# Performance work log

Measured on AMD Instinct MI355X. Metric: run time of the kernel, lower is better.

The kernel has to match this reference:

```python
import jax, jax.numpy as jnp
import numpy as np

B, N, S = 8, 4096, 1024
D1, D2 = 128, 256
IN_C = D1 + D2
MLP = [256, 256]
BN_EPS = 1e-5


def setup_inputs() -> dict:
    key = jax.random.key(0)
    ks = jax.random.split(key, 32)
    inp = {
        'xyz1': jax.random.uniform(ks[0], (B, 3, N), dtype=jnp.float32),
        'xyz2': jax.random.uniform(ks[1], (B, 3, S), dtype=jnp.float32),
        'points1': jax.random.normal(ks[2], (B, D1, N), dtype=jnp.float32),
        'points2': jax.random.normal(ks[3], (B, D2, S), dtype=jnp.float32),
        'colors1': jax.random.normal(ks[4], (B, D1, N), dtype=jnp.float32),
        'colors2': jax.random.normal(ks[5], (B, D2, S), dtype=jnp.float32),
    }
    # conv1x1 + BN params for the two MLP stacks (points / colors)
    k = 6
    last = IN_C
    for li, out_c in enumerate(MLP, start=1):
        for tag in ('p', 'c'):
            scale = 1.0 / np.sqrt(last)
            inp[f'W{tag}{li}'] = jax.random.uniform(ks[k], (out_c, last), jnp.float32, -scale, scale); k += 1
            inp[f'b{tag}{li}'] = jax.random.uniform(ks[k], (out_c,), jnp.float32, -scale, scale); k += 1
            inp[f'g{tag}{li}'] = jnp.ones((out_c,), jnp.float32)
            inp[f'be{tag}{li}'] = jnp.zeros((out_c,), jnp.float32)
        last = out_c
    return inp


def _square_distance(src, dst):
    # src [B,N,3], dst [B,S,3] -> [B,N,S]
    d = -2.0 * jnp.einsum('bnc,bsc->bns', src, dst)
    d = d + jnp.sum(src * src, -1)[:, :, None]
    d = d + jnp.sum(dst * dst, -1)[:, None, :]
    return d


def _three_interp(xyz1, xyz2, feat2):
    # xyz1 [B,N,3], xyz2 [B,S,3], feat2 [B,S,D] -> [B,N,D]
    dists = _square_distance(xyz1, xyz2)              # [B,N,S]
    neg_d3, idx = jax.lax.top_k(-dists, 3)            # smallest 3 distances
    d3 = -neg_d3                                      # [B,N,3] ascending
    recip = 1.0 / (d3 + 1e-8)
    weight = recip / jnp.sum(recip, axis=2, keepdims=True)
    gathered = jax.vmap(lambda f, i: f[i])(feat2, idx)  # [B,N,3,D]
    return jnp.sum(gathered * weight[..., None], axis=2)


def _conv_bn_relu(x, W, b, g, be):
    # x [B,N,Cin]; conv1x1 == per-point linear; BN in training mode (batch stats)
    y = jnp.einsum('bnc,oc->bno', x, W) + b
    m = jnp.mean(y, axis=(0, 1))
    v = jnp.var(y, axis=(0, 1))
    yn = (y - m) * jax.lax.rsqrt(v + BN_EPS)
    return jax.nn.relu(yn * g + be)


def reference(xyz1, xyz2, points1, points2, colors1, colors2,
              Wp1, bp1, gp1, bep1, Wc1, bc1, gc1, bec1,
              Wp2, bp2, gp2, bep2, Wc2, bc2, gc2, bec2):
    x1 = jnp.transpose(xyz1, (0, 2, 1))   # [B,N,3]
    x2 = jnp.transpose(xyz2, (0, 2, 1))   # [B,S,3]
    p2 = jnp.transpose(points2, (0, 2, 1))  # [B,S,D2]
    c2 = jnp.transpose(colors2, (0, 2, 1))

    interp_p = _three_interp(x1, x2, p2)  # [B,N,D2]
    interp_c = _three_interp(x1, x2, c2)

    p1 = jnp.transpose(points1, (0, 2, 1))  # [B,N,D1]
    c1 = jnp.transpose(colors1, (0, 2, 1))
    new_p = jnp.concatenate([p1, interp_p], axis=-1)  # [B,N,IN_C]
    new_c = jnp.concatenate([c1, interp_c], axis=-1)

    new_p = _conv_bn_relu(new_p, Wp1, bp1, gp1, bep1)
    new_p = _conv_bn_relu(new_p, Wp2, bp2, gp2, bep2)
    new_c = _conv_bn_relu(new_c, Wc1, bc1, gc1, bec1)
    new_c = _conv_bn_relu(new_c, Wc2, bc2, gc2, bec2)

    return (jnp.transpose(new_p, (0, 2, 1)), jnp.transpose(new_c, (0, 2, 1)))
```

## Files before the change

kernel.cpp:

```cpp
#include <hip/hip_runtime.h>
#include <cstdint>
#include <cstddef>


#define B_   8
#define N_   4096
#define S_   1024
#define D1_  128
#define D2_  256
#define INC_ 384
#define OC_  256
#define M_   (B_ * N_)

typedef __attribute__((ext_vector_type(8))) short sh8;
typedef __attribute__((ext_vector_type(4))) float f32x4;
typedef __attribute__((ext_vector_type(4))) unsigned short ush4;
typedef __attribute__((ext_vector_type(8))) unsigned short ush8;

__device__ __forceinline__ unsigned short bf16rne(float f) {
    union { float f; unsigned u; } v; v.f = f;
    return (unsigned short)((v.u + 0x7FFFu + ((v.u >> 16) & 1u)) >> 16);
}
__device__ __forceinline__ float bf2f(unsigned short h) {
    union { unsigned u; float f; } v; v.u = ((unsigned)h) << 16;
    return v.f;
}
__device__ __forceinline__ void gload16(const void* gsrc, void* lds) {
    __builtin_amdgcn_global_load_lds(
        (const __attribute__((address_space(1))) void*)gsrc,
        (__attribute__((address_space(3))) void*)lds, 16, 0, 0);
}

#define INS(pd, pi) { \
    bool l0 = (pd < d0) || (pd == d0 && pi < i0); \
    bool l1 = (pd < d1) || (pd == d1 && pi < i1); \
    bool l2 = (pd < d2) || (pd == d2 && pi < i2); \
    d2 = l1 ? d1 : (l2 ? pd : d2);  i2 = l1 ? i1 : (l2 ? pi : i2); \
    d1 = l0 ? d0 : (l1 ? pd : d1);  i1 = l0 ? i0 : (l1 ? pi : i1); \
    d0 = l0 ? pd : d0;              i0 = l0 ? pi : i0; \
}

__global__ __launch_bounds__(256) void front_kernel(
    const float* __restrict__ xyz1, const float* __restrict__ xyz2,
    const float* __restrict__ points1, const float* __restrict__ colors1,
    const float* __restrict__ points2, const float* __restrict__ colors2,
    const float* __restrict__ Wp1, const float* __restrict__ Wc1,
    const float* __restrict__ Wp2, const float* __restrict__ Wc2,
    int* __restrict__ idxo, float* __restrict__ wo,
    unsigned short* __restrict__ p2b, unsigned short* __restrict__ c2b,
    unsigned short* __restrict__ Wb1, unsigned short* __restrict__ Wb2,
    unsigned short* __restrict__ Xp)
{
    __shared__ __align__(16) char fsm[17664];
    const int bid = blockIdx.x;
    const int tid = threadIdx.x;

    if (bid < 1024) {
        float4* sc = (float4*)fsm;
        const int b = bid >> 7, qb = bid & 127;
        const float* x2 = xyz2 + (size_t)b * 3 * S_;
        for (int s = tid; s < S_; s += 256) {
            float xs = x2[s], ys = x2[S_ + s], zs = x2[2 * S_ + s];
            sc[s] = make_float4(xs, ys, zs, xs * xs + ys * ys + zs * zs);
        }
        __syncthreads();
        const int q = qb * 32 + (tid >> 3);
        const int sub = tid & 7;
        const float* x1 = xyz1 + (size_t)b * 3 * N_;
        const float xq = x1[q], yq = x1[N_ + q], zq = x1[2 * N_ + q];
        const float n1 = xq * xq + yq * yq + zq * zq;
        float d0 = 3.4e38f, d1 = 3.4e38f, d2 = 3.4e38f;
        int i0 = 0, i1 = 0, i2 = 0;
#pragma unroll 4
        for (int j = 0; j < 128; ++j) {
            int s = j * 8 + sub;
            float4 v = sc[s];
            float dot = xq * v.x + yq * v.y + zq * v.z;
            float d = (n1 - 2.0f * dot) + v.w;
            bool c0 = d < d0, c1 = d < d1, c2 = d < d2;
            d2 = c1 ? d1 : (c2 ? d : d2); i2 = c1 ? i1 : (c2 ? s : i2);
            d1 = c0 ? d0 : (c1 ? d : d1); i1 = c0 ? i0 : (c1 ? s : i1);
            d0 = c0 ? d : d0;             i0 = c0 ? s : i0;
        }
#pragma unroll
        for (int off = 1; off < 8; off <<= 1) {
            float pd0 = __shfl_xor(d0, off), pd1 = __shfl_xor(d1, off), pd2 = __shfl_xor(d2, off);
            int   pi0 = __shfl_xor(i0, off), pi1 = __shfl_xor(i1, off), pi2 = __shfl_xor(i2, off);
            INS(pd0, pi0) INS(pd1, pi1) INS(pd2, pi2)
        }
        if (sub == 0) {
            float r0 = 1.f / (d0 + 1e-8f);
            float r1 = 1.f / (d1 + 1e-8f);
            float r2 = 1.f / (d2 + 1e-8f);
            float rs = r0 + r1 + r2;
            int base = (b * N_ + q) * 3;
            idxo[base] = i0; idxo[base + 1] = i1; idxo[base + 2] = i2;
            wo[base] = r0 / rs; wo[base + 1] = r1 / rs; wo[base + 2] = r2 / rs;
        }
    } else if (bid < 1536) {
        float (*tile)[33] = (float(*)[33])fsm;
        const int u = bid - 1024;
        const int which = u >> 8;
        const int v = u & 255;
        const int z = v >> 5, cx = v & 31;
        const int tx = tid & 31, ty = tid >> 5;
        const float* s = (which ? colors2 : points2) + (size_t)z * D2_ * S_;
        unsigned short* d = (which ? c2b : p2b) + (size_t)z * S_ * D2_;
        for (int ry = 0; ry < 8; ++ry) {
            if (ry) __syncthreads();
#pragma unroll
            for (int i = 0; i < 4; ++i)
                tile[ty + i * 8][tx] = s[(size_t)(ry * 32 + ty + i * 8) * S_ + cx * 32 + tx];
            __syncthreads();
#pragma unroll
            for (int i = 0; i < 4; ++i)
                d[(size_t)(cx * 32 + ty + i * 8) * D2_ + ry * 32 + tx] =
                    bf16rne(tile[tx][ty + i * 8]);
        }
    } else if (bid < 1856) {
        int e = ((bid - 1536) * 256 + tid) * 4;
        const float* src; unsigned short* dst; int off;
        if (e < 98304)       { src = Wp1; dst = Wb1;          off = e; }
        else if (e < 196608) { src = Wc1; dst = Wb1 + 98304;  off = e - 98304; }
        else if (e < 262144) { src = Wp2; dst = Wb2;          off = e - 196608; }
        else                 { src = Wc2; dst = Wb2 + 65536;  off = e - 262144; }
        float4 v = *(const float4*)(src + off);
        ush4 o; o[0] = bf16rne(v.x); o[1] = bf16rne(v.y); o[2] = bf16rne(v.z); o[3] = bf16rne(v.w);
        *(ush4*)(dst + off) = o;
    } else {
        float (*tileA)[69] = (float(*)[69])fsm;
        const int u = bid - 1856;
        const int t = u >> 9, rem = u & 511;
        const int b = rem >> 6, n0 = (rem & 63) * 64;
        const float* x1 = t ? colors1 : points1;
        size_t mbase = (size_t)t * M_ + (size_t)b * N_ + n0;
#pragma unroll
        for (int ph = 0; ph < 2; ++ph) {
            if (ph) __syncthreads();
#pragma unroll
            for (int it = 0; it < 4; ++it) {
                int fl4 = it * 256 + tid;
                int dl = fl4 >> 4, nl = (fl4 & 15) * 4;
                float4 v = *(const float4*)(x1 + ((size_t)b * D1_ + ph * 64 + dl) * N_ + n0 + nl);
                tileA[nl][dl] = v.x; tileA[nl + 1][dl] = v.y;
                tileA[nl + 2][dl] = v.z; tileA[nl + 3][dl] = v.w;
            }
            __syncthreads();
#pragma unroll
            for (int it = 0; it < 2; ++it) {
                int e8 = it * 256 + tid;
                int r = e8 >> 3, dc = (e8 & 7) * 8;
                ush8 o;
#pragma unroll
                for (int j = 0; j < 8; ++j) o[j] = bf16rne(tileA[r][dc + j]);
                *(ush8*)(Xp + (mbase + r) * D1_ + ph * 64 + dc) = o;
            }
        }
    }
}

__global__ __launch_bounds__(512, 1) void gemm1f_kernel(
    const unsigned short* __restrict__ Xp,
    const unsigned short* __restrict__ p2b,
    const unsigned short* __restrict__ c2b,
    const int* __restrict__ idxw, const float* __restrict__ wgtw,
    const unsigned short* __restrict__ Wb1,
    unsigned short* __restrict__ Y1,
    float* __restrict__ psum, float* __restrict__ psq)
{
    const int wg  = blockIdx.x;
    const int xcd = wg & 7;
    const int t   = xcd & 1;
    const int mt  = (xcd >> 1) * 32 + (wg >> 3);
    const int m0  = mt * 256;
    const int bb  = m0 >> 12;
    const unsigned short* Aw  = Wb1 + (size_t)t * (OC_ * INC_);
    const unsigned short* Xb  = Xp + (size_t)t * M_ * D1_;
    const unsigned short* f2b = t ? c2b : p2b;

    __shared__ __align__(16) char smem[131072];

    const int tid  = threadIdx.x;
    const int lane = tid & 63;
    const int wid  = tid >> 6;
    const int wc   = wid & 3;
    const int wm   = wid >> 2;
    const int srow = tid >> 3;
    const int k8   = (tid & 7) * 8;
    const int sk   = ((tid & 7) ^ (srow & 7)) * 8;
    const int kgrp = (lane >> 4) * 16;

    int gi[4][3]; float gw[4][3];
#pragma unroll
    for (int p = 0; p < 4; ++p) {
        int base = (m0 + p * 64 + srow) * 3;
#pragma unroll
        for (int j = 0; j < 3; ++j) { gi[p][j] = idxw[base + j]; gw[p][j] = wgtw[base + j]; }
    }

    f32x4 acc[4][8];
#pragma unroll
    for (int i = 0; i < 4; ++i)
#pragma unroll
        for (int j = 0; j < 8; ++j) acc[i][j] = f32x4{0.f, 0.f, 0.f, 0.f};

    auto stageA = [&](int buf, int kc) {
#pragma unroll
        for (int p = 0; p < 4; ++p)
            gload16(Aw + (size_t)(p * 64 + srow) * INC_ + kc + sk,
                    smem + buf * 32768 + p * 8192 + wid * 1024);
    };
    auto stageBX = [&](int buf, int kc) {
#pragma unroll
        for (int p = 0; p < 4; ++p)
            gload16(Xb + (size_t)(m0 + p * 64 + srow) * D1_ + kc + sk,
                    smem + 65536 + buf * 32768 + p * 8192 + wid * 1024);
    };
    auto stageBG = [&](int buf, int kc) {
        const int d0k = kc - D1_ + k8;
#pragma unroll
        for (int p = 0; p < 4; ++p) {
            int row = p * 64 + srow;
            ush8 a0 = *(const ush8*)(f2b + ((size_t)bb * S_ + gi[p][0]) * D2_ + d0k);
            ush8 a1 = *(const ush8*)(f2b + ((size_t)bb * S_ + gi[p][1]) * D2_ + d0k);
            ush8 a2 = *(const ush8*)(f2b + ((size_t)bb * S_ + gi[p][2]) * D2_ + d0k);
            ush8 ov;
#pragma unroll
            for (int j = 0; j < 8; ++j)
                ov[j] = bf16rne(gw[p][0] * bf2f(a0[j]) + gw[p][1] * bf2f(a1[j])
                              + gw[p][2] * bf2f(a2[j]));
            *(ush8*)(smem + 65536 + buf * 32768 + row * 128
                     + ((k8 * 2) ^ ((row & 7) << 4))) = ov;
        }
    };
    auto compute = [&](int buf) {
#pragma unroll
        for (int kk = 0; kk < 2; ++kk) {
            sh8 a[4], b[8];
#pragma unroll
            for (int f = 0; f < 4; ++f) {
                int ra = wc * 64 + (lane & 15) + f * 16;
                a[f] = *(const sh8*)(smem + buf * 32768 + ra * 128
                        + ((kk * 64 + kgrp) ^ ((ra & 7) << 4)));
            }
#pragma unroll
            for (int f = 0; f < 8; ++f) {
                int rb = wm * 128 + (lane & 15) + f * 16;
                b[f] = *(const sh8*)(smem + 65536 + buf * 32768 + rb * 128
                        + ((kk * 64 + kgrp) ^ ((rb & 7) << 4)));
            }
#pragma unroll
            for (int fc = 0; fc < 4; ++fc)
#pragma unroll
                for (int fm = 0; fm < 8; ++fm)
                    acc[fc][fm] = __builtin_amdgcn_mfma_f32_16x16x32_bf16(
                        a[fc], b[fm], acc[fc][fm], 0, 0, 0);
        }
    };

    stageA(0, 0); stageBX(0, 0);
    __syncthreads();
    int cur = 0;
    for (int step = 0; step < 6; ++step) {
        int kcn = (step + 1) * 64;
        if (step < 5) {
            stageA(cur ^ 1, kcn);
            if (kcn < D1_) stageBX(cur ^ 1, kcn);
            else           stageBG(cur ^ 1, kcn);
        }
        compute(cur);
        __syncthreads();
        cur ^= 1;
    }

    const int mrow = m0 + wm * 128 + (lane & 15);
    const int chq  = (lane >> 4) * 4;
#pragma unroll
    for (int fm = 0; fm < 8; ++fm)
#pragma unroll
        for (int fc = 0; fc < 4; ++fc) {
            ush4 v;
#pragma unroll
            for (int r = 0; r < 4; ++r) v[r] = bf16rne(acc[fc][fm][r]);
            *(ush4*)(Y1 + ((size_t)t * M_ + mrow + fm * 16) * OC_
                      + wc * 64 + fc * 16 + chq) = v;
        }

    float* sArr = (float*)smem;
    const int contrib = wm * 16 + (lane & 15);
#pragma unroll
    for (int ph = 0; ph < 2; ++ph) {
#pragma unroll
        for (int fc = 0; fc < 4; ++fc) {
            f32x4 s4;
#pragma unroll
            for (int r = 0; r < 4; ++r) {
                float s = 0.f;
#pragma unroll
                for (int fm = 0; fm < 8; ++fm) { float v = acc[fc][fm][r]; s += ph ? v * v : v; }
                s4[r] = s;
            }
            *(f32x4*)&sArr[contrib * 264 + wc * 64 + fc * 16 + chq] = s4;
        }
        __syncthreads();
        if (tid < 256) {
            float s = 0.f;
#pragma unroll
            for (int k = 0; k < 32; ++k) s += sArr[((k + tid) & 31) * 264 + tid];
            (ph ? psq : psum)[((size_t)t * 128 + mt) * 256 + tid] = s;
        }
        __syncthreads();
    }
}

__global__ __launch_bounds__(256) void reduce_kernel(
    const float* __restrict__ psum, const float* __restrict__ psq,
    const float* __restrict__ gp, const float* __restrict__ bep,
    const float* __restrict__ gc, const float* __restrict__ bec,
    float* __restrict__ ss, int layerOff)
{
    const int t = blockIdx.x, cs = blockIdx.y;
    const int tid = threadIdx.x;
    const int cl = tid & 63, grp = tid >> 6;
    const int c = cs * 64 + cl;
    float s = 0.f, q = 0.f;
    for (int k = grp; k < 128; k += 4) {
        s += psum[((size_t)t * 128 + k) * 256 + c];
        q += psq [((size_t)t * 128 + k) * 256 + c];
    }
    __shared__ float ls[4][64], lq[4][64];
    ls[grp][cl] = s; lq[grp][cl] = q;
    __syncthreads();
    if (tid < 64) {
        s = ls[0][cl] + ls[1][cl] + ls[2][cl] + ls[3][cl];
        q = lq[0][cl] + lq[1][cl] + lq[2][cl] + lq[3][cl];
        float mean = s * (1.f / (float)M_);
        float var  = q * (1.f / (float)M_) - mean * mean;
        float inv  = rsqrtf(var + 1e-5f);
        float g = (t ? gc : gp)[c], be = (t ? bec : bep)[c];
        float sc = g * inv;
        ss[layerOff + t * 256 + c]       = sc;
        ss[layerOff + 512 + t * 256 + c] = be - mean * sc;
    }
}

__global__ __launch_bounds__(512, 1) void gemm2f_kernel(
    const unsigned short* __restrict__ Y1,
    const unsigned short* __restrict__ Wb2,
    const float* __restrict__ ss,
    unsigned short* __restrict__ y2b,
    float* __restrict__ psum, float* __restrict__ psq)
{
    const int wg  = blockIdx.x;
    const int xcd = wg & 7;
    const int t   = xcd & 1;
    const int mt  = (xcd >> 1) * 32 + (wg >> 3);
    const int m0  = mt * 256;
    const unsigned short* Aw = Wb2 + (size_t)t * (OC_ * OC_);
    const unsigned short* By = Y1 + (size_t)t * M_ * OC_;

    __shared__ __align__(16) char smem[131072];
    __shared__ float Slds[256], Hlds[256];

    const int tid  = threadIdx.x;
    const int lane = tid & 63;
    const int wid  = tid >> 6;
    const int wc   = wid & 3;
    const int wm   = wid >> 2;
    const int srow = tid >> 3;
    const int k8   = (tid & 7) * 8;
    const int sk   = ((tid & 7) ^ (srow & 7)) * 8;
    const int kgrp = (lane >> 4) * 16;

    if (tid < 256) { Slds[tid] = ss[t * 256 + tid]; Hlds[tid] = ss[512 + t * 256 + tid]; }
    __syncthreads();

    f32x4 acc[4][8];
#pragma unroll
    for (int i = 0; i < 4; ++i)
#pragma unroll
        for (int j = 0; j < 8; ++j) acc[i][j] = f32x4{0.f, 0.f, 0.f, 0.f};

    auto stageA = [&](int buf, int kc) {
#pragma unroll
        for (int p = 0; p < 4; ++p)
            gload16(Aw + (size_t)(p * 64 + srow) * OC_ + kc + sk,
                    smem + buf * 32768 + p * 8192 + wid * 1024);
    };
    auto stageBY = [&](int buf, int kc) {
#pragma unroll
        for (int p = 0; p < 4; ++p) {
            int row = p * 64 + srow;
            ush8 yv = *(const ush8*)(By + (size_t)(m0 + row) * OC_ + kc + k8);
            ush8 ov;
#pragma unroll
            for (int j = 0; j < 8; ++j) {
                float y = bf2f(yv[j]);
                ov[j] = bf16rne(fmaxf(0.f, fmaf(y, Slds[kc + k8 + j], Hlds[kc + k8 + j])));
            }
            *(ush8*)(smem + 65536 + buf * 32768 + row * 128
                     + ((k8 * 2) ^ ((row & 7) << 4))) = ov;
        }
    };
    auto compute = [&](int buf) {
#pragma unroll
        for (int kk = 0; kk < 2; ++kk) {
            sh8 a[4], b[8];
#pragma unroll
            for (int f = 0; f < 4; ++f) {
                int ra = wc * 64 + (lane & 15) + f * 16;
                a[f] = *(const sh8*)(smem + buf * 32768 + ra * 128
                        + ((kk * 64 + kgrp) ^ ((ra & 7) << 4)));
            }
#pragma unroll
            for (int f = 0; f < 8; ++f) {
                int rb = wm * 128 + (lane & 15) + f * 16;
                b[f] = *(const sh8*)(smem + 65536 + buf * 32768 + rb * 128
                        + ((kk * 64 + kgrp) ^ ((rb & 7) << 4)));
            }
#pragma unroll
            for (int fc = 0; fc < 4; ++fc)
#pragma unroll
                for (int fm = 0; fm < 8; ++fm)
                    acc[fc][fm] = __builtin_amdgcn_mfma_f32_16x16x32_bf16(
                        a[fc], b[fm], acc[fc][fm], 0, 0, 0);
        }
    };

    stageA(0, 0); stageBY(0, 0);
    __syncthreads();
    int cur = 0;
    for (int step = 0; step < 4; ++step) {
        int kcn = (step + 1) * 64;
        if (step < 3) { stageA(cur ^ 1, kcn); stageBY(cur ^ 1, kcn); }
        compute(cur);
        __syncthreads();
        cur ^= 1;
    }

    const int mrow = m0 + wm * 128 + (lane & 15);
    const int chq  = (lane >> 4) * 4;
#pragma unroll
    for (int fm = 0; fm < 8; ++fm)
#pragma unroll
        for (int fc = 0; fc < 4; ++fc) {
            ush4 v;
#pragma unroll
            for (int r = 0; r < 4; ++r) v[r] = bf16rne(acc[fc][fm][r]);
            *(ush4*)(y2b + ((size_t)t * M_ + mrow + fm * 16) * OC_
                      + wc * 64 + fc * 16 + chq) = v;
        }

    float* sArr = (float*)smem;
    const int contrib = wm * 16 + (lane & 15);
#pragma unroll
    for (int ph = 0; ph < 2; ++ph) {
#pragma unroll
        for (int fc = 0; fc < 4; ++fc) {
            f32x4 s4;
#pragma unroll
            for (int r = 0; r < 4; ++r) {
                float s = 0.f;
#pragma unroll
                for (int fm = 0; fm < 8; ++fm) { float v = acc[fc][fm][r]; s += ph ? v * v : v; }
                s4[r] = s;
            }
            *(f32x4*)&sArr[contrib * 264 + wc * 64 + fc * 16 + chq] = s4;
        }
        __syncthreads();
        if (tid < 256) {
            float s = 0.f;
#pragma unroll
            for (int k = 0; k < 32; ++k) s += sArr[((k + tid) & 31) * 264 + tid];
            (ph ? psq : psum)[((size_t)t * 128 + mt) * 256 + tid] = s;
        }
        __syncthreads();
    }
}

__global__ __launch_bounds__(256) void bnT_kernel(
    const unsigned short* __restrict__ y2b, const float* __restrict__ ss,
    float* __restrict__ out)
{
    const int z = blockIdx.z;
    const int t = z >> 3, b = z & 7;
    const int o0 = blockIdx.y * 64;
    const int n0 = blockIdx.x * 64;
    const int tid = threadIdx.x;
    __shared__ unsigned short tile[64][72];

    const unsigned short* src = y2b + ((size_t)t * M_ + (size_t)b * N_ + n0) * OC_ + o0;
#pragma unroll
    for (int it = 0; it < 2; ++it) {
        int u = it * 256 + tid;
        int m_l = u >> 3, o8 = (u & 7) * 8;
        *(ush8*)&tile[m_l][o8] = *(const ush8*)(src + (size_t)m_l * OC_ + o8);
    }
    __syncthreads();
#pragma unroll
    for (int it = 0; it < 4; ++it) {
        int v = it * 256 + tid;
        int o_l = v >> 4, n4 = (v & 15) * 4;
        int o = o0 + o_l;
        float sc = ss[1024 + t * 256 + o];
        float sh = ss[1536 + t * 256 + o];
        float4 w;
        w.x = fmaxf(0.f, fmaf(bf2f(tile[n4][o_l]),     sc, sh));
        w.y = fmaxf(0.f, fmaf(bf2f(tile[n4 + 1][o_l]), sc, sh));
        w.z = fmaxf(0.f, fmaf(bf2f(tile[n4 + 2][o_l]), sc, sh));
        w.w = fmaxf(0.f, fmaf(bf2f(tile[n4 + 3][o_l]), sc, sh));
        *(float4*)(out + (((size_t)t * B_ + b) * OC_ + o) * N_ + n0 + n4) = w;
    }
}

extern "C" void kernel_launch(void* const* d_in, const int* in_sizes, int n_in,
                              void* d_out, int out_size, void* d_ws, size_t ws_size,
                              hipStream_t stream)
{
    const float* xyz1    = (const float*)d_in[0];
    const float* xyz2    = (const float*)d_in[1];
    const float* points1 = (const float*)d_in[2];
    const float* points2 = (const float*)d_in[3];
    const float* colors1 = (const float*)d_in[4];
    const float* colors2 = (const float*)d_in[5];
    const float* Wp1  = (const float*)d_in[6];
    const float* gp1  = (const float*)d_in[8];
    const float* bep1 = (const float*)d_in[9];
    const float* Wc1  = (const float*)d_in[10];
    const float* gc1  = (const float*)d_in[12];
    const float* bec1 = (const float*)d_in[13];
    const float* Wp2  = (const float*)d_in[14];
    const float* gp2  = (const float*)d_in[16];
    const float* bep2 = (const float*)d_in[17];
    const float* Wc2  = (const float*)d_in[18];
    const float* gc2  = (const float*)d_in[20];
    const float* bec2 = (const float*)d_in[21];

    char* ws = (char*)d_ws;
    unsigned short* y2b  = (unsigned short*)(ws + 0);
    unsigned short* Xp   = (unsigned short*)(ws + 0);
    unsigned short* p2b  = (unsigned short*)(ws + 16777216);
    unsigned short* c2b  = (unsigned short*)(ws + 20971520);
    int*   idxw = (int*)  (ws + 25165824);
    float* wgtw = (float*)(ws + 25559040);
    unsigned short* Y1   = (unsigned short*)(ws + 33554432);
    unsigned short* Wb1  = (unsigned short*)(ws + 67108864);
    unsigned short* Wb2  = (unsigned short*)(ws + 67895296);
    float* psum = (float*)(ws + 68419584);
    float* psq  = (float*)(ws + 68681728);
    float* ssb  = (float*)(ws + 68943872);
    float* out  = (float*)d_out;

    front_kernel<<<2880, 256, 0, stream>>>(xyz1, xyz2, points1, colors1,
                                           points2, colors2, Wp1, Wc1, Wp2, Wc2,
                                           idxw, wgtw, p2b, c2b, Wb1, Wb2, Xp);
    gemm1f_kernel<<<256, 512, 0, stream>>>(Xp, p2b, c2b, idxw, wgtw,
                                           Wb1, Y1, psum, psq);
    reduce_kernel<<<dim3(2, 4), 256, 0, stream>>>(psum, psq, gp1, bep1, gc1, bec1, ssb, 0);
    gemm2f_kernel<<<256, 512, 0, stream>>>(Y1, Wb2, ssb, y2b, psum, psq);
    reduce_kernel<<<dim3(2, 4), 256, 0, stream>>>(psum, psq, gp2, bep2, gc2, bec2, ssb, 1024);
    bnT_kernel<<<dim3(64, 4, 16), 256, 0, stream>>>(y2b, ssb, out);
}
```

Baseline: 114.4 us.

## Single-buffer GEMM LDS for two blocks per CU; two queries per KNN thread

Measured after the change: 120.6 us. 5.4% more time.

```diff
diff --git a/kernel.cpp b/kernel.cpp
--- a/kernel.cpp
+++ b/kernel.cpp
@@ -31,7 +31,7 @@
         (__attribute__((address_space(3))) void*)lds, 16, 0, 0);
 }
 
-#define INS(pd, pi) { \
+#define INS(pd, pi, d0, d1, d2, i0, i1, i2) { \
     bool l0 = (pd < d0) || (pd == d0 && pi < i0); \
     bool l1 = (pd < d1) || (pd == d1 && pi < i1); \
     bool l2 = (pd < d2) || (pd == d2 && pi < i2); \
@@ -55,51 +55,77 @@
     const int bid = blockIdx.x;
     const int tid = threadIdx.x;
 
-    if (bid < 1024) {
+    if (bid < 512) {
         float4* sc = (float4*)fsm;
-        const int b = bid >> 7, qb = bid & 127;
+        const int b = bid >> 6, qb = bid & 63;
         const float* x2 = xyz2 + (size_t)b * 3 * S_;
         for (int s = tid; s < S_; s += 256) {
             float xs = x2[s], ys = x2[S_ + s], zs = x2[2 * S_ + s];
             sc[s] = make_float4(xs, ys, zs, xs * xs + ys * ys + zs * zs);
         }
         __syncthreads();
-        const int q = qb * 32 + (tid >> 3);
+        const int qA = qb * 64 + (tid >> 3);
+        const int qB = qA + 32;
         const int sub = tid & 7;
         const float* x1 = xyz1 + (size_t)b * 3 * N_;
-        const float xq = x1[q], yq = x1[N_ + q], zq = x1[2 * N_ + q];
-        const float n1 = xq * xq + yq * yq + zq * zq;
-        float d0 = 3.4e38f, d1 = 3.4e38f, d2 = 3.4e38f;
-        int i0 = 0, i1 = 0, i2 = 0;
+        const float xa = x1[qA], ya = x1[N_ + qA], za = x1[2 * N_ + qA];
+        const float xb = x1[qB], yb = x1[N_ + qB], zb = x1[2 * N_ + qB];
+        const float na = xa * xa + ya * ya + za * za;
+        const float nb = xb * xb + yb * yb + zb * zb;
+        float ad0 = 3.4e38f, ad1 = 3.4e38f, ad2 = 3.4e38f;
+        float bd0 = 3.4e38f, bd1 = 3.4e38f, bd2 = 3.4e38f;
+        int ai0 = 0, ai1 = 0, ai2 = 0, bi0 = 0, bi1 = 0, bi2 = 0;
 #pragma unroll 4
         for (int j = 0; j < 128; ++j) {
             int s = j * 8 + sub;
             float4 v = sc[s];
-            float dot = xq * v.x + yq * v.y + zq * v.z;
-            float d = (n1 - 2.0f * dot) + v.w;
-            bool c0 = d < d0, c1 = d < d1, c2 = d < d2;
-            d2 = c1 ? d1 : (c2 ? d : d2); i2 = c1 ? i1 : (c2 ? s : i2);
-            d1 = c0 ? d0 : (c1 ? d : d1); i1 = c0 ? i0 : (c1 ? s : i1);
-            d0 = c0 ? d : d0;             i0 = c0 ? s : i0;
+            float da = (na - 2.0f * (xa * v.x + ya * v.y + za * v.z)) + v.w;
+            float db = (nb - 2.0f * (xb * v.x + yb * v.y + zb * v.z)) + v.w;
+            bool a0 = da < ad0, a1 = da < ad1, a2 = da < ad2;
+            ad2 = a1 ? ad1 : (a2 ? da : ad2); ai2 = a1 ? ai1 : (a2 ? s : ai2);
+            ad1 = a0 ? ad0 : (a1 ? da : ad1); ai1 = a0 ? ai0 : (a1 ? s : ai1);
+            ad0 = a0 ? da : ad0;              ai0 = a0 ? s : ai0;
+            bool b0 = db < bd0, b1 = db < bd1, b2 = db < bd2;
+            bd2 = b1 ? bd1 : (b2 ? db : bd2); bi2 = b1 ? bi1 : (b2 ? s : bi2);
+            bd1 = b0 ? bd0 : (b1 ? db : bd1); bi1 = b0 ? bi0 : (b1 ? s : bi1);
+            bd0 = b0 ? db : bd0;              bi0 = b0 ? s : bi0;
         }
 #pragma unroll
         for (int off = 1; off < 8; off <<= 1) {
-            float pd0 = __shfl_xor(d0, off), pd1 = __shfl_xor(d1, off), pd2 = __shfl_xor(d2, off);
-            int   pi0 = __shfl_xor(i0, off), pi1 = __shfl_xor(i1, off), pi2 = __shfl_xor(i2, off);
-            INS(pd0, pi0) INS(pd1, pi1) INS(pd2, pi2)
+            float p0 = __shfl_xor(ad0, off), p1 = __shfl_xor(ad1, off), p2 = __shfl_xor(ad2, off);
+            int   j0 = __shfl_xor(ai0, off), j1 = __shfl_xor(ai1, off), j2 = __shfl_xor(ai2, off);
+            INS(p0, j0, ad0, ad1, ad2, ai0, ai1, ai2)
+            INS(p1, j1, ad0, ad1, ad2, ai0, ai1, ai2)
+            INS(p2, j2, ad0, ad1, ad2, ai0, ai1, ai2)
+            float q0 = __shfl_xor(bd0, off), q1 = __shfl_xor(bd1, off), q2 = __shfl_xor(bd2, off);
+            int   k0 = __shfl_xor(bi0, off), k1 = __shfl_xor(bi1, off), k2 = __shfl_xor(bi2, off);
+            INS(q0, k0, bd0, bd1, bd2, bi0, bi1, bi2)
+            INS(q1, k1, bd0, bd1, bd2, bi0, bi1, bi2)
+            INS(q2, k2, bd0, bd1, bd2, bi0, bi1, bi2)
         }
         if (sub == 0) {
-            float r0 = 1.f / (d0 + 1e-8f);
-            float r1 = 1.f / (d1 + 1e-8f);
-            float r2 = 1.f / (d2 + 1e-8f);
-            float rs = r0 + r1 + r2;
-            int base = (b * N_ + q) * 3;
-            idxo[base] = i0; idxo[base + 1] = i1; idxo[base + 2] = i2;
-            wo[base] = r0 / rs; wo[base + 1] = r1 / rs; wo[base + 2] = r2 / rs;
-        }
-    } else if (bid < 1536) {
+            {
+                float r0 = 1.f / (ad0 + 1e-8f);
+                float r1 = 1.f / (ad1 + 1e-8f);
+                float r2 = 1.f / (ad2 + 1e-8f);
+                float rs = r0 + r1 + r2;
+                int base = (b * N_ + qA) * 3;
+                idxo[base] = ai0; idxo[base + 1] = ai1; idxo[base + 2] = ai2;
+                wo[base] = r0 / rs; wo[base + 1] = r1 / rs; wo[base + 2] = r2 / rs;
+            }
+            {
+                float r0 = 1.f / (bd0 + 1e-8f);
+                float r1 = 1.f / (bd1 + 1e-8f);
+                float r2 = 1.f / (bd2 + 1e-8f);
+                float rs = r0 + r1 + r2;
+                int base = (b * N_ + qB) * 3;
+                idxo[base] = bi0; idxo[base + 1] = bi1; idxo[base + 2] = bi2;
+                wo[base] = r0 / rs; wo[base + 1] = r1 / rs; wo[base + 2] = r2 / rs;
+            }
+        }
+    } else if (bid < 1024) {
         float (*tile)[33] = (float(*)[33])fsm;
-        const int u = bid - 1024;
+        const int u = bid - 512;
         const int which = u >> 8;
         const int v = u & 255;
         const int z = v >> 5, cx = v & 31;
@@ -117,8 +143,8 @@
                 d[(size_t)(cx * 32 + ty + i * 8) * D2_ + ry * 32 + tx] =
                     bf16rne(tile[tx][ty + i * 8]);
         }
-    } else if (bid < 1856) {
-        int e = ((bid - 1536) * 256 + tid) * 4;
+    } else if (bid < 1344) {
+        int e = ((bid - 1024) * 256 + tid) * 4;
         const float* src; unsigned short* dst; int off;
         if (e < 98304)       { src = Wp1; dst = Wb1;          off = e; }
         else if (e < 196608) { src = Wc1; dst = Wb1 + 98304;  off = e - 98304; }
@@ -129,7 +155,7 @@
         *(ush4*)(dst + off) = o;
     } else {
         float (*tileA)[69] = (float(*)[69])fsm;
-        const int u = bid - 1856;
+        const int u = bid - 1344;
         const int t = u >> 9, rem = u & 511;
         const int b = rem >> 6, n0 = (rem & 63) * 64;
         const float* x1 = t ? colors1 : points1;
@@ -159,7 +185,7 @@
     }
 }
 
-__global__ __launch_bounds__(512, 1) void gemm1f_kernel(
+__global__ __launch_bounds__(512, 2) void gemm1f_kernel(
     const unsigned short* __restrict__ Xp,
     const unsigned short* __restrict__ p2b,
     const unsigned short* __restrict__ c2b,
@@ -178,7 +204,7 @@
     const unsigned short* Xb  = Xp + (size_t)t * M_ * D1_;
     const unsigned short* f2b = t ? c2b : p2b;
 
-    __shared__ __align__(16) char smem[131072];
+    __shared__ __align__(16) char smem[65536];
 
     const int tid  = threadIdx.x;
     const int lane = tid & 63;
@@ -204,19 +230,19 @@
 #pragma unroll
         for (int j = 0; j < 8; ++j) acc[i][j] = f32x4{0.f, 0.f, 0.f, 0.f};
 
-    auto stageA = [&](int buf, int kc) {
+    auto stageA = [&](int kc) {
 #pragma unroll
         for (int p = 0; p < 4; ++p)
             gload16(Aw + (size_t)(p * 64 + srow) * INC_ + kc + sk,
-                    smem + buf * 32768 + p * 8192 + wid * 1024);
-    };
-    auto stageBX = [&](int buf, int kc) {
+                    smem + p * 8192 + wid * 1024);
+    };
+    auto stageBX = [&](int kc) {
 #pragma unroll
         for (int p = 0; p < 4; ++p)
             gload16(Xb + (size_t)(m0 + p * 64 + srow) * D1_ + kc + sk,
-                    smem + 65536 + buf * 32768 + p * 8192 + wid * 1024);
-    };
-    auto stageBG = [&](int buf, int kc) {
+                    smem + 32768 + p * 8192 + wid * 1024);
+    };
+    auto stageBG = [&](int kc) {
         const int d0k = kc - D1_ + k8;
 #pragma unroll
         for (int p = 0; p < 4; ++p) {
@@ -229,24 +255,23 @@
             for (int j = 0; j < 8; ++j)
                 ov[j] = bf16rne(gw[p][0] * bf2f(a0[j]) + gw[p][1] * bf2f(a1[j])
                               + gw[p][2] * bf2f(a2[j]));
-            *(ush8*)(smem + 65536 + buf * 32768 + row * 128
-                     + ((k8 * 2) ^ ((row & 7) << 4))) = ov;
-        }
-    };
-    auto compute = [&](int buf) {
+            *(ush8*)(smem + 32768 + row * 128 + ((k8 * 2) ^ ((row & 7) << 4))) = ov;
+        }
+    };
+    auto compute = [&]() {
 #pragma unroll
         for (int kk = 0; kk < 2; ++kk) {
             sh8 a[4], b[8];
 #pragma unroll
             for (int f = 0; f < 4; ++f) {
                 int ra = wc * 64 + (lane & 15) + f * 16;
-                a[f] = *(const sh8*)(smem + buf * 32768 + ra * 128
+                a[f] = *(const sh8*)(smem + ra * 128
                         + ((kk * 64 + kgrp) ^ ((ra & 7) << 4)));
             }
 #pragma unroll
             for (int f = 0; f < 8; ++f) {
                 int rb = wm * 128 + (lane & 15) + f * 16;
-                b[f] = *(const sh8*)(smem + 65536 + buf * 32768 + rb * 128
+                b[f] = *(const sh8*)(smem + 32768 + rb * 128
                         + ((kk * 64 + kgrp) ^ ((rb & 7) << 4)));
             }
 #pragma unroll
@@ -258,20 +283,16 @@
         }
     };
 
-    stageA(0, 0); stageBX(0, 0);
+    for (int step = 0; step < 6; ++step) {
+        int kc = step * 64;
+        if (step) __syncthreads();
+        stageA(kc);
+        if (kc < D1_) stageBX(kc);
+        else          stageBG(kc);
+        __syncthreads();
+        compute();
+    }
     __syncthreads();
-    int cur = 0;
-    for (int step = 0; step < 6; ++step) {
-        int kcn = (step + 1) * 64;
-        if (step < 5) {
-            stageA(cur ^ 1, kcn);
-            if (kcn < D1_) stageBX(cur ^ 1, kcn);
-            else           stageBG(cur ^ 1, kcn);
-        }
-        compute(cur);
-        __syncthreads();
-        cur ^= 1;
-    }
 
     const int mrow = m0 + wm * 128 + (lane & 15);
     const int chq  = (lane >> 4) * 4;
@@ -344,7 +365,7 @@
     }
 }
 
-__global__ __launch_bounds__(512, 1) void gemm2f_kernel(
+__global__ __launch_bounds__(512, 2) void gemm2f_kernel(
     const unsigned short* __restrict__ Y1,
     const unsigned short* __restrict__ Wb2,
     const float* __restrict__ ss,
@@ -359,7 +380,7 @@
     const unsigned short* Aw = Wb2 + (size_t)t * (OC_ * OC_);
     const unsigned short* By = Y1 + (size_t)t * M_ * OC_;
 
-    __shared__ __align__(16) char smem[131072];
+    __shared__ __align__(16) char smem[65536];
     __shared__ float Slds[256], Hlds[256];
 
     const int tid  = threadIdx.x;
@@ -381,13 +402,13 @@
 #pragma unroll
         for (int j = 0; j < 8; ++j) acc[i][j] = f32x4{0.f, 0.f, 0.f, 0.f};
 
-    auto stageA = [&](int buf, int kc) {
+    auto stageA = [&](int kc) {
 #pragma unroll
         for (int p = 0; p < 4; ++p)
             gload16(Aw + (size_t)(p * 64 + srow) * OC_ + kc + sk,
-                    smem + buf * 32768 + p * 8192 + wid * 1024);
-    };
-    auto stageBY = [&](int buf, int kc) {
+                    smem + p * 8192 + wid * 1024);
+    };
+    auto stageBY = [&](int kc) {
 #pragma unroll
         for (int p = 0; p < 4; ++p) {
             int row = p * 64 + srow;
@@ -398,24 +419,23 @@
                 float y = bf2f(yv[j]);
                 ov[j] = bf16rne(fmaxf(0.f, fmaf(y, Slds[kc + k8 + j], Hlds[kc + k8 + j])));
             }
-            *(ush8*)(smem + 65536 + buf * 32768 + row * 128
-                     + ((k8 * 2) ^ ((row & 7) << 4))) = ov;
-        }
-    };
-    auto compute = [&](int buf) {
+            *(ush8*)(smem + 32768 + row * 128 + ((k8 * 2) ^ ((row & 7) << 4))) = ov;
+        }
+    };
+    auto compute = [&]() {
 #pragma unroll
         for (int kk = 0; kk < 2; ++kk) {
             sh8 a[4], b[8];
 #pragma unroll
             for (int f = 0; f < 4; ++f) {
                 int ra = wc * 64 + (lane & 15) + f * 16;
-                a[f] = *(const sh8*)(smem + buf * 32768 + ra * 128
+                a[f] = *(const sh8*)(smem + ra * 128
                         + ((kk * 64 + kgrp) ^ ((ra & 7) << 4)));
             }
 #pragma unroll
             for (int f = 0; f < 8; ++f) {
                 int rb = wm * 128 + (lane & 15) + f * 16;
-                b[f] = *(const sh8*)(smem + 65536 + buf * 32768 + rb * 128
+                b[f] = *(const sh8*)(smem + 32768 + rb * 128
                         + ((kk * 64 + kgrp) ^ ((rb & 7) << 4)));
             }
 #pragma unroll
@@ -427,16 +447,15 @@
         }
     };
 
-    stageA(0, 0); stageBY(0, 0);
+    for (int step = 0; step < 4; ++step) {
+        int kc = step * 64;
+        if (step) __syncthreads();
+        stageA(kc);
+        stageBY(kc);
+        __syncthreads();
+        compute();
+    }
     __syncthreads();
-    int cur = 0;
-    for (int step = 0; step < 4; ++step) {
-        int kcn = (step + 1) * 64;
-        if (step < 3) { stageA(cur ^ 1, kcn); stageBY(cur ^ 1, kcn); }
-        compute(cur);
-        __syncthreads();
-        cur ^= 1;
-    }
 
     const int mrow = m0 + wm * 128 + (lane & 15);
     const int chq  = (lane >> 4) * 4;
@@ -551,7 +570,7 @@
     float* ssb  = (float*)(ws + 68943872);
     float* out  = (float*)d_out;
 
-    front_kernel<<<2880, 256, 0, stream>>>(xyz1, xyz2, points1, colors1,
+    front_kernel<<<2368, 256, 0, stream>>>(xyz1, xyz2, points1, colors1,
                                            points2, colors2, Wp1, Wc1, Wp2, Wc2,
                                            idxw, wgtw, p2b, c2b, Wb1, Wb2, Xp);
     gemm1f_kernel<<<256, 512, 0, stream>>>(Xp, p2b, c2b, idxw, wgtw,
```
